# Optimization experiments

Measured on AMD Instinct MI355X. Metric: run time of the kernel, lower is better.

Reference implementation:

```python
import jax, jax.numpy as jnp
import numpy as np

B, LQ, LK, D, H = 2, 1024, 1024, 1024, 16
DH = D // H


def setup_inputs() -> dict:
    key = jax.random.key(0)
    ks = jax.random.split(key, 14)
    s = 1.0 / np.sqrt(D)
    inp = {
        "q": jax.random.normal(ks[0], (B, LQ, D), jnp.float32),
        "k": jax.random.normal(ks[1], (B, LK, D), jnp.float32),
        "v": jax.random.normal(ks[2], (B, LK, D), jnp.float32),
        "Wq": jax.random.normal(ks[3], (D, D), jnp.float32) * s,
        "bq": jnp.zeros((D,), jnp.float32),
        "Wk": jax.random.normal(ks[4], (D, D), jnp.float32) * s,
        "bk": jnp.zeros((D,), jnp.float32),
        "Wv": jax.random.normal(ks[5], (D, D), jnp.float32) * s,
        "bv": jnp.zeros((D,), jnp.float32),
        "Wo": jax.random.normal(ks[6], (D, D), jnp.float32) * s,
        "bo": jnp.zeros((D,), jnp.float32),
        "logits_bias": jax.random.normal(ks[7], (B, LQ, LK), jnp.float32),
        "key_padding_mask": jax.random.randint(ks[8], (B, LK), 0, 2) > 0,
    }
    return inp


def _split_heads(x):
    b, l, _ = x.shape
    return x.reshape(b, l, H, DH).transpose(0, 2, 1, 3)  # [B,H,L,DH]


def reference(q, k, v, Wq, bq, Wk, bk, Wv, bv, Wo, bo, logits_bias, key_padding_mask):
    qh = _split_heads(q @ Wq.T + bq)  # [B,H,Lq,DH]
    kh = _split_heads(k @ Wk.T + bk)  # [B,H,Lk,DH]
    vh = _split_heads(v @ Wv.T + bv)  # [B,H,Lk,DH]

    neg = jnp.finfo(qh.dtype).min
    # attn_mask = logits_bias broadcast over heads, masked_fill at padded keys
    attn_mask = jnp.where(key_padding_mask[:, None, None, :],
                          neg, logits_bias[:, None, :, :])  # [B,1,Lq,Lk]

    scale = 1.0 / np.sqrt(DH)
    scores = jnp.einsum('bhqd,bhkd->bhqk', qh, kh) * scale + attn_mask
    probs = jax.nn.softmax(scores, axis=-1)
    out = jnp.einsum('bhqk,bhkd->bhqd', probs, vh)  # [B,H,Lq,DH]
    out = out.transpose(0, 2, 1, 3).reshape(q.shape[0], q.shape[1], D)
    return out @ Wo.T + bo
```

## Files before the change

### kernel.cpp

```cpp
#include <hip/hip_runtime.h>


typedef _Float16 half8 __attribute__((ext_vector_type(8)));
typedef _Float16 half4_t __attribute__((ext_vector_type(4)));
typedef float f32x4 __attribute__((ext_vector_type(4)));

#define MFMA16(a, b, c) __builtin_amdgcn_mfma_f32_16x16x32_f16((a), (b), (c), 0, 0, 0)

#define WAITCNT_VM(n) asm volatile("s_waitcnt vmcnt(" #n ")" ::: "memory")
#define WAITCNT_LGKM0() asm volatile("s_waitcnt lgkmcnt(0)" ::: "memory")
#define RAW_BARRIER() asm volatile("s_barrier" ::: "memory")

__device__ __forceinline__ void gload16(const void* g, void* l) {
  __builtin_amdgcn_global_load_lds(
      (const __attribute__((address_space(1))) unsigned int*)g,
      (__attribute__((address_space(3))) unsigned int*)l, 16, 0, 0);
}

__device__ __forceinline__ half8 frag_ld(const _Float16* t, int row, int ck) {
  return *(const half8*)(t + row * 64 + (((ck ^ (row & 7)) << 3)));
}

__global__ __launch_bounds__(256) void cvt_f32_f16(
    const float* __restrict__ q, const float* __restrict__ k, const float* __restrict__ v,
    const float* __restrict__ Wq, const float* __restrict__ Wk,
    const float* __restrict__ Wv, const float* __restrict__ Wo,
    _Float16* __restrict__ q16, _Float16* __restrict__ k16, _Float16* __restrict__ v16,
    _Float16* __restrict__ w16) {
  const int y = blockIdx.y;
  if (y >= 3 && blockIdx.x >= 512) return;
  const float* s;
  _Float16* d;
  const size_t M = (size_t)1024 * 1024;
  switch (y) {
    case 0: s = q;  d = q16; break;
    case 1: s = k;  d = k16; break;
    case 2: s = v;  d = v16; break;
    case 3: s = Wq; d = w16; break;
    case 4: s = Wk; d = w16 + M; break;
    case 5: s = Wv; d = w16 + 2 * M; break;
    default: s = Wo; d = w16 + 3 * M; break;
  }
  const size_t i = ((size_t)blockIdx.x * 256 + threadIdx.x) * 8;
  const float4 a = *(const float4*)(s + i);
  const float4 bvv = *(const float4*)(s + i + 4);
  half8 h;
  h[0] = (_Float16)a.x; h[1] = (_Float16)a.y; h[2] = (_Float16)a.z; h[3] = (_Float16)a.w;
  h[4] = (_Float16)bvv.x; h[5] = (_Float16)bvv.y; h[6] = (_Float16)bvv.z; h[7] = (_Float16)bvv.w;
  *(half8*)(d + i) = h;
}

__global__ __launch_bounds__(256) void mmp(
    const _Float16* __restrict__ Aq, const _Float16* __restrict__ Ak,
    const _Float16* __restrict__ Av, const _Float16* __restrict__ W16,
    const float* __restrict__ c0, const float* __restrict__ c1,
    const float* __restrict__ c2, _Float16* __restrict__ Dq,
    _Float16* __restrict__ Dk, _Float16* __restrict__ Dvt,
    float* __restrict__ Df, int is_final) {
  __shared__ __align__(16) _Float16 lds[24576];

  const int tid = threadIdx.x;
  const int wv = tid >> 6, ln = tid & 63;
  const int quad = ln >> 4, col = ln & 15;
  const int wm = wv >> 1, wn = wv & 1;
  const int n0 = blockIdx.x * 128;
  const int m0 = blockIdx.y * 64;
  const int z = blockIdx.z;

  const _Float16* A = (z == 0) ? Aq : (z == 1) ? Ak : Av;
  const _Float16* Bw = W16 + (size_t)z * 1024 * 1024;
  const float* bias = (z == 0) ? c0 : (z == 1) ? c1 : c2;

  auto stage = [&](int buf, int k0) {
#pragma unroll
    for (int j = 0; j < 6; ++j) {
      const int ci = j * 256 + tid;
      const _Float16* src;
      if (ci < 512) {
        const int row = ci >> 3, lc = (ci & 7) ^ (row & 7);
        src = A + (size_t)(m0 + row) * 1024 + k0 + lc * 8;
      } else {
        const int di = ci - 512;
        const int row = di >> 3, lc = (di & 7) ^ (row & 7);
        src = Bw + (size_t)(n0 + row) * 1024 + k0 + lc * 8;
      }
      gload16(src, lds + buf * 12288 + (j * 256 + wv * 64) * 8);
    }
  };

  const f32x4 zero4 = {0.f, 0.f, 0.f, 0.f};
  f32x4 acc[2][4];
#pragma unroll
  for (int i = 0; i < 2; ++i)
#pragma unroll
    for (int j = 0; j < 4; ++j) acc[i][j] = zero4;

  stage(0, 0);
  for (int i = 0; i < 15; ++i) {
    stage((i + 1) & 1, (i + 1) * 64);
    WAITCNT_VM(6);
    RAW_BARRIER();
    const _Float16* As = lds + (i & 1) * 12288;
    const _Float16* Bs = As + 4096;
    half8 af[2][2], bf[2][4];
#pragma unroll
    for (int kk = 0; kk < 2; ++kk) {
#pragma unroll
      for (int mi = 0; mi < 2; ++mi)
        af[kk][mi] = frag_ld(As, wm * 32 + mi * 16 + col, kk * 4 + quad);
#pragma unroll
      for (int ni = 0; ni < 4; ++ni)
        bf[kk][ni] = frag_ld(Bs, wn * 64 + ni * 16 + col, kk * 4 + quad);
    }
    WAITCNT_LGKM0();
    RAW_BARRIER();
#pragma unroll
    for (int kk = 0; kk < 2; ++kk)
#pragma unroll
      for (int mi = 0; mi < 2; ++mi)
#pragma unroll
        for (int ni = 0; ni < 4; ++ni)
          acc[mi][ni] = MFMA16(af[kk][mi], bf[kk][ni], acc[mi][ni]);
  }
  {
    WAITCNT_VM(0);
    RAW_BARRIER();
    const _Float16* As = lds + 12288;
    const _Float16* Bs = As + 4096;
#pragma unroll
    for (int kk = 0; kk < 2; ++kk) {
      half8 af[2], bf[4];
#pragma unroll
      for (int mi = 0; mi < 2; ++mi)
        af[mi] = frag_ld(As, wm * 32 + mi * 16 + col, kk * 4 + quad);
#pragma unroll
      for (int ni = 0; ni < 4; ++ni)
        bf[ni] = frag_ld(Bs, wn * 64 + ni * 16 + col, kk * 4 + quad);
#pragma unroll
      for (int mi = 0; mi < 2; ++mi)
#pragma unroll
        for (int ni = 0; ni < 4; ++ni)
          acc[mi][ni] = MFMA16(af[mi], bf[ni], acc[mi][ni]);
    }
  }

  float bv[4];
#pragma unroll
  for (int ni = 0; ni < 4; ++ni) bv[ni] = bias[n0 + wn * 64 + ni * 16 + col];

  if (is_final) {
#pragma unroll
    for (int mi = 0; mi < 2; ++mi) {
      const int m_g = m0 + wm * 32 + mi * 16 + quad * 4;
#pragma unroll
      for (int ni = 0; ni < 4; ++ni) {
        const int n_g = n0 + wn * 64 + ni * 16 + col;
#pragma unroll
        for (int r = 0; r < 4; ++r)
          Df[(size_t)(m_g + r) * 1024 + n_g] = acc[mi][ni][r] + bv[ni];
      }
    }
  } else if (z < 2) {
    _Float16* D = z ? Dk : Dq;
#pragma unroll
    for (int mi = 0; mi < 2; ++mi) {
      const int m_g = m0 + wm * 32 + mi * 16 + quad * 4;
#pragma unroll
      for (int ni = 0; ni < 4; ++ni) {
        const int n_g = n0 + wn * 64 + ni * 16 + col;
        const int h = n_g >> 6, dh = n_g & 63;
#pragma unroll
        for (int r = 0; r < 4; ++r) {
          const int b = (m_g + r) >> 10, l = (m_g + r) & 1023;
          D[((size_t)((b * 16 + h) * 1024) + l) * 64 + dh] =
              (_Float16)(acc[mi][ni][r] + bv[ni]);
        }
      }
    }
  } else {
    __syncthreads();
    _Float16* Ct = lds;
#pragma unroll
    for (int mi = 0; mi < 2; ++mi) {
      const int ml = wm * 32 + mi * 16 + quad * 4;
#pragma unroll
      for (int ni = 0; ni < 4; ++ni) {
        const int nl = wn * 64 + ni * 16 + col;
#pragma unroll
        for (int r = 0; r < 4; ++r)
          Ct[(size_t)nl * 72 + ml + r] = (_Float16)(acc[mi][ni][r] + bv[ni]);
      }
    }
    __syncthreads();
#pragma unroll
    for (int it = 0; it < 4; ++it) {
      const int ci = it * 256 + tid;
      const int n = ci >> 3;
      const int mc = (ci & 7) * 8;
      const half8 hv = *(const half8*)(Ct + (size_t)n * 72 + mc);
      const int n_g = n0 + n;
      const int h = n_g >> 6, dh = n_g & 63;
      const int m_g = m0 + mc;
      const int b = m_g >> 10, l = m_g & 1023;
      *(half8*)(Dvt + ((size_t)((b * 16 + h) * 64 + dh)) * 1024 + l) = hv;
    }
  }
}

__global__ __launch_bounds__(256) void attn(
    const _Float16* __restrict__ Qh, const _Float16* __restrict__ Kh,
    const _Float16* __restrict__ Vt, const float* __restrict__ biasL,
    const int* __restrict__ kpm, _Float16* __restrict__ AO) {
  __shared__ __align__(16) _Float16 KV[2 * 16384];
  __shared__ __align__(16) _Float16 Pt[4][1024];

  const int tid = threadIdx.x;
  const int wv = tid >> 6, ln = tid & 63;
  const int quad = ln >> 4, col = ln & 15;
  const int qsub = wv & 1, khalf = wv >> 1;
  const int q0 = blockIdx.x * 32;
  const int bh = blockIdx.y;
  const int b = bh >> 4, hh = bh & 15;
  const int qg = q0 + qsub * 16 + col;

  const _Float16* Qp = Qh + ((size_t)bh * 1024 + qg) * 64;
  const half8 bq0 = *(const half8*)(Qp + quad * 8);
  const half8 bq1 = *(const half8*)(Qp + 32 + quad * 8);
  WAITCNT_VM(0);

  const float* biasRow = biasL + ((size_t)(b * 1024 + qg)) * 1024;
  const int* kpmRow = kpm + b * 1024;
  const int stage_kbase = (wv & 1) * 512;

  auto stageKV = [&](int buf, int it) {
    const int skoff = stage_kbase + it * 64;
#pragma unroll
    for (int j = 0; j < 8; ++j) {
      const int ci = j * 64 + ln;
      const int row = ci >> 3;
      const int lc = (ci & 7) ^ (row & 7);
      const void* src =
          (wv < 2) ? (const void*)(Kh + ((size_t)bh * 1024 + skoff + row) * 64 + lc * 8)
                   : (const void*)(Vt + ((size_t)bh * 64 + row) * 1024 + skoff + lc * 8);
      gload16(src, KV + buf * 16384 + wv * 4096 + j * 512);
    }
  };
  auto loadBias = [&](int it, f32x4* bb, int4* mk) {
    const int koff = khalf * 512 + it * 64;
#pragma unroll
    for (int mi = 0; mi < 4; ++mi) {
      const int kg = koff + mi * 16 + quad * 4;
      mk[mi] = *(const int4*)&kpmRow[kg];
      bb[mi] = *(const f32x4*)&biasRow[kg];
    }
  };

  const f32x4 zero4 = {0.f, 0.f, 0.f, 0.f};
  f32x4 o[4];
#pragma unroll
  for (int ni = 0; ni < 4; ++ni) o[ni] = zero4;
  float m_i = -1e30f, l_i = 0.f;
  _Float16* Pw = Pt[wv];

  auto compute = [&](int buf, const f32x4* bb, const int4* mk) {
    const _Float16* Ks = KV + buf * 16384 + khalf * 4096;
    const _Float16* Vs = KV + buf * 16384 + (2 + khalf) * 4096;
    f32x4 s[4];
#pragma unroll
    for (int mi = 0; mi < 4; ++mi) {
      f32x4 a4 = zero4;
      a4 = MFMA16(frag_ld(Ks, mi * 16 + col, quad), bq0, a4);
      a4 = MFMA16(frag_ld(Ks, mi * 16 + col, 4 + quad), bq1, a4);
      s[mi] = a4;
    }
#pragma unroll
    for (int mi = 0; mi < 4; ++mi) {
      const int* mp = (const int*)&mk[mi];
#pragma unroll
      for (int r = 0; r < 4; ++r)
        s[mi][r] = mp[r] ? -1e9f : s[mi][r] * 0.125f + bb[mi][r];
    }
    float rm = -1e30f;
#pragma unroll
    for (int mi = 0; mi < 4; ++mi)
#pragma unroll
      for (int r = 0; r < 4; ++r) rm = fmaxf(rm, s[mi][r]);
    rm = fmaxf(rm, __shfl_xor(rm, 16));
    rm = fmaxf(rm, __shfl_xor(rm, 32));
    const float mn = fmaxf(m_i, rm);
    const float alpha = __expf(m_i - mn);
    m_i = mn;
    float ps = 0.f;
#pragma unroll
    for (int mi = 0; mi < 4; ++mi)
#pragma unroll
      for (int r = 0; r < 4; ++r) {
        const float p = __expf(s[mi][r] - mn);
        s[mi][r] = p;
        ps += p;
      }
    ps += __shfl_xor(ps, 16);
    ps += __shfl_xor(ps, 32);
    l_i = l_i * alpha + ps;
#pragma unroll
    for (int ni = 0; ni < 4; ++ni)
#pragma unroll
      for (int r = 0; r < 4; ++r) o[ni][r] *= alpha;
#pragma unroll
    for (int mi = 0; mi < 4; ++mi) {
      half4_t h;
      h[0] = (_Float16)s[mi][0]; h[1] = (_Float16)s[mi][1];
      h[2] = (_Float16)s[mi][2]; h[3] = (_Float16)s[mi][3];
      const int kloc = mi * 16 + quad * 4;
      const int chunk = kloc >> 3;
      *(half4_t*)(Pw + col * 64 + (((chunk ^ (col & 7)) << 3) | (kloc & 7))) = h;
    }
    const half8 p0 = frag_ld(Pw, col, quad);
    const half8 p1 = frag_ld(Pw, col, 4 + quad);
#pragma unroll
    for (int ni = 0; ni < 4; ++ni) {
      o[ni] = MFMA16(frag_ld(Vs, ni * 16 + col, quad), p0, o[ni]);
      o[ni] = MFMA16(frag_ld(Vs, ni * 16 + col, 4 + quad), p1, o[ni]);
    }
  };

  f32x4 bbA[4], bbB[4];
  int4 mkA[4], mkB[4];
  stageKV(0, 0);
  loadBias(0, bbA, mkA);
  for (int i = 0; i < 7; ++i) {
    stageKV((i + 1) & 1, i + 1);
    loadBias(i + 1, bbB, mkB);
    WAITCNT_VM(16);
    RAW_BARRIER();
    compute(i & 1, bbA, mkA);
    WAITCNT_LGKM0();
    RAW_BARRIER();
#pragma unroll
    for (int mi = 0; mi < 4; ++mi) { bbA[mi] = bbB[mi]; mkA[mi] = mkB[mi]; }
  }
  WAITCNT_VM(0);
  RAW_BARRIER();
  compute(1, bbA, mkA);

  __syncthreads();
  f32x4* Ox = (f32x4*)&Pt[0][0];
  float* MlS = (float*)&KV[0];
  if (khalf == 1) {
#pragma unroll
    for (int ni = 0; ni < 4; ++ni) Ox[(qsub * 4 + ni) * 64 + ln] = o[ni];
    MlS[qsub * 64 + ln] = m_i;
    MlS[128 + qsub * 64 + ln] = l_i;
  }
  __syncthreads();
  if (khalf == 0) {
    const float m2 = MlS[qsub * 64 + ln];
    const float l2 = MlS[128 + qsub * 64 + ln];
    const float ms = fmaxf(m_i, m2);
    const float w1 = __expf(m_i - ms);
    const float w2 = __expf(m2 - ms);
    const float inv = 1.0f / (l_i * w1 + l2 * w2);
#pragma unroll
    for (int ni = 0; ni < 4; ++ni) {
      const f32x4 o2 = Ox[(qsub * 4 + ni) * 64 + ln];
      half4_t h;
#pragma unroll
      for (int r = 0; r < 4; ++r)
        h[r] = (_Float16)((o[ni][r] * w1 + o2[r] * w2) * inv);
      *(half4_t*)&AO[((size_t)(b * 1024 + qg)) * 1024 + hh * 64 + ni * 16 + quad * 4] = h;
    }
  }
}

extern "C" void kernel_launch(void* const* d_in, const int* in_sizes, int n_in,
                              void* d_out, int out_size, void* d_ws, size_t ws_size,
                              hipStream_t stream) {
  (void)in_sizes; (void)n_in; (void)out_size; (void)ws_size;
  const float* q = (const float*)d_in[0];
  const float* k = (const float*)d_in[1];
  const float* v = (const float*)d_in[2];
  const float* Wq = (const float*)d_in[3];
  const float* bq = (const float*)d_in[4];
  const float* Wk = (const float*)d_in[5];
  const float* bk = (const float*)d_in[6];
  const float* Wv = (const float*)d_in[7];
  const float* bv = (const float*)d_in[8];
  const float* Wo = (const float*)d_in[9];
  const float* bo = (const float*)d_in[10];
  const float* lb = (const float*)d_in[11];
  const int* kpm = (const int*)d_in[12];
  float* out = (float*)d_out;

  const size_t NT = (size_t)2 * 1024 * 1024;
  _Float16* q16 = (_Float16*)d_ws;
  _Float16* k16 = q16 + NT;
  _Float16* v16 = k16 + NT;
  _Float16* Qh = v16 + NT;
  _Float16* Kh = Qh + NT;
  _Float16* Vt = Kh + NT;
  _Float16* w16 = Vt + NT;
  _Float16* AO = q16;

  cvt_f32_f16<<<dim3(1024, 7), 256, 0, stream>>>(q, k, v, Wq, Wk, Wv, Wo,
                                                 q16, k16, v16, w16);
  mmp<<<dim3(8, 32, 3), 256, 0, stream>>>(q16, k16, v16, w16, bq, bk, bv,
                                          Qh, Kh, Vt, nullptr, 0);
  attn<<<dim3(32, 32), 256, 0, stream>>>(Qh, Kh, Vt, lb, kpm, AO);
  mmp<<<dim3(8, 32, 1), 256, 0, stream>>>(AO, nullptr, nullptr, w16 + 3 * NT / 2,
                                          bo, nullptr, nullptr, nullptr, nullptr,
                                          nullptr, out, 1);
}
```

Baseline: 177.5 us.

## Precompute fp16 masked bias in log2 domain and restructure attention to 512-thread blocks

Adds a pre-pass that folds the key-padding mask and a log2(e) scale into an fp16 bias tensor, so the attention loop reads half the bias bytes and no mask. Attention now uses exp2 with a pre-scaled QK factor. Blocks grow to 512 threads covering 64 queries, split keys within each 64-key tile, and share one K/V stage per iteration. The cost is an extra kernel pass over the full bias and fp16 rounding of the bias.

```diff
diff --git a/kernel.cpp b/kernel.cpp
--- a/kernel.cpp
+++ b/kernel.cpp
@@ -10,6 +10,7 @@
 #define WAITCNT_VM(n) asm volatile("s_waitcnt vmcnt(" #n ")" ::: "memory")
 #define WAITCNT_LGKM0() asm volatile("s_waitcnt lgkmcnt(0)" ::: "memory")
 #define RAW_BARRIER() asm volatile("s_barrier" ::: "memory")
+#define EXP2F(x) __builtin_amdgcn_exp2f(x)
 
 __device__ __forceinline__ void gload16(const void* g, void* l) {
   __builtin_amdgcn_global_load_lds(
@@ -50,6 +51,30 @@
   *(half8*)(d + i) = h;
 }
 
+__global__ __launch_bounds__(256) void cvt_bias(
+    const float* __restrict__ biasL, const int* __restrict__ kpm,
+    _Float16* __restrict__ biasC) {
+  const size_t i = ((size_t)blockIdx.x * 256 + threadIdx.x) * 8;
+  const int b = (int)(i >> 20);
+  const int kk = (int)(i & 1023);
+  const int* mrow = kpm + (b << 10) + kk;
+  const float4 b0 = *(const float4*)(biasL + i);
+  const float4 b1 = *(const float4*)(biasL + i + 4);
+  const int4 m0 = *(const int4*)mrow;
+  const int4 m1 = *(const int4*)(mrow + 4);
+  const float sc = 1.44269504f;
+  half8 h;
+  h[0] = m0.x ? (_Float16)-30000.f : (_Float16)(b0.x * sc);
+  h[1] = m0.y ? (_Float16)-30000.f : (_Float16)(b0.y * sc);
+  h[2] = m0.z ? (_Float16)-30000.f : (_Float16)(b0.z * sc);
+  h[3] = m0.w ? (_Float16)-30000.f : (_Float16)(b0.w * sc);
+  h[4] = m1.x ? (_Float16)-30000.f : (_Float16)(b1.x * sc);
+  h[5] = m1.y ? (_Float16)-30000.f : (_Float16)(b1.y * sc);
+  h[6] = m1.z ? (_Float16)-30000.f : (_Float16)(b1.z * sc);
+  h[7] = m1.w ? (_Float16)-30000.f : (_Float16)(b1.w * sc);
+  *(half8*)(biasC + i) = h;
+}
+
 __global__ __launch_bounds__(256) void mmp(
     const _Float16* __restrict__ Aq, const _Float16* __restrict__ Ak,
     const _Float16* __restrict__ Av, const _Float16* __restrict__ W16,
@@ -207,18 +232,18 @@
   }
 }
 
-__global__ __launch_bounds__(256) void attn(
+__global__ __launch_bounds__(512, 4) void attn(
     const _Float16* __restrict__ Qh, const _Float16* __restrict__ Kh,
-    const _Float16* __restrict__ Vt, const float* __restrict__ biasL,
-    const int* __restrict__ kpm, _Float16* __restrict__ AO) {
-  __shared__ __align__(16) _Float16 KV[2 * 16384];
-  __shared__ __align__(16) _Float16 Pt[4][1024];
+    const _Float16* __restrict__ Vt, const _Float16* __restrict__ biasC,
+    _Float16* __restrict__ AO) {
+  __shared__ __align__(16) _Float16 KV[2 * 8192];
+  __shared__ __align__(16) _Float16 Pt[8][512];
 
   const int tid = threadIdx.x;
   const int wv = tid >> 6, ln = tid & 63;
   const int quad = ln >> 4, col = ln & 15;
-  const int qsub = wv & 1, khalf = wv >> 1;
-  const int q0 = blockIdx.x * 32;
+  const int qsub = wv >> 1, khalf = wv & 1;
+  const int q0 = blockIdx.x * 64;
   const int bh = blockIdx.y;
   const int b = bh >> 4, hh = bh & 15;
   const int qg = q0 + qsub * 16 + col;
@@ -228,31 +253,30 @@
   const half8 bq1 = *(const half8*)(Qp + 32 + quad * 8);
   WAITCNT_VM(0);
 
-  const float* biasRow = biasL + ((size_t)(b * 1024 + qg)) * 1024;
-  const int* kpmRow = kpm + b * 1024;
-  const int stage_kbase = (wv & 1) * 512;
+  const _Float16* biasRow = biasC + ((size_t)(b * 1024 + qg)) * 1024;
 
   auto stageKV = [&](int buf, int it) {
-    const int skoff = stage_kbase + it * 64;
-#pragma unroll
-    for (int j = 0; j < 8; ++j) {
-      const int ci = j * 64 + ln;
-      const int row = ci >> 3;
-      const int lc = (ci & 7) ^ (row & 7);
-      const void* src =
-          (wv < 2) ? (const void*)(Kh + ((size_t)bh * 1024 + skoff + row) * 64 + lc * 8)
-                   : (const void*)(Vt + ((size_t)bh * 64 + row) * 1024 + skoff + lc * 8);
-      gload16(src, KV + buf * 16384 + wv * 4096 + j * 512);
+    const int koff = it * 64;
+#pragma unroll
+    for (int j = 0; j < 2; ++j) {
+      const int ci = j * 512 + tid;
+      const void* src;
+      if (ci < 512) {
+        const int row = ci >> 3, lc = (ci & 7) ^ (row & 7);
+        src = Kh + ((size_t)bh * 1024 + koff + row) * 64 + lc * 8;
+      } else {
+        const int di = ci - 512;
+        const int row = di >> 3, lc = (di & 7) ^ (row & 7);
+        src = Vt + ((size_t)bh * 64 + row) * 1024 + koff + lc * 8;
+      }
+      gload16(src, KV + buf * 8192 + (j * 512 + wv * 64) * 8);
     }
   };
-  auto loadBias = [&](int it, f32x4* bb, int4* mk) {
-    const int koff = khalf * 512 + it * 64;
-#pragma unroll
-    for (int mi = 0; mi < 4; ++mi) {
-      const int kg = koff + mi * 16 + quad * 4;
-      mk[mi] = *(const int4*)&kpmRow[kg];
-      bb[mi] = *(const f32x4*)&biasRow[kg];
-    }
+  auto loadBias = [&](int it, half4_t* bb) {
+    const int koff = it * 64 + khalf * 32;
+#pragma unroll
+    for (int mi = 0; mi < 2; ++mi)
+      bb[mi] = *(const half4_t*)&biasRow[koff + mi * 16 + quad * 4];
   };
 
   const f32x4 zero4 = {0.f, 0.f, 0.f, 0.f};
@@ -262,40 +286,35 @@
   float m_i = -1e30f, l_i = 0.f;
   _Float16* Pw = Pt[wv];
 
-  auto compute = [&](int buf, const f32x4* bb, const int4* mk) {
-    const _Float16* Ks = KV + buf * 16384 + khalf * 4096;
-    const _Float16* Vs = KV + buf * 16384 + (2 + khalf) * 4096;
-    f32x4 s[4];
-#pragma unroll
-    for (int mi = 0; mi < 4; ++mi) {
+  auto compute = [&](int buf, const half4_t* bb) {
+    const _Float16* Ks = KV + buf * 8192;
+    const _Float16* Vs = Ks + 4096;
+    f32x4 s[2];
+#pragma unroll
+    for (int mi = 0; mi < 2; ++mi) {
       f32x4 a4 = zero4;
-      a4 = MFMA16(frag_ld(Ks, mi * 16 + col, quad), bq0, a4);
-      a4 = MFMA16(frag_ld(Ks, mi * 16 + col, 4 + quad), bq1, a4);
+      a4 = MFMA16(frag_ld(Ks, khalf * 32 + mi * 16 + col, quad), bq0, a4);
+      a4 = MFMA16(frag_ld(Ks, khalf * 32 + mi * 16 + col, 4 + quad), bq1, a4);
       s[mi] = a4;
     }
 #pragma unroll
-    for (int mi = 0; mi < 4; ++mi) {
-      const int* mp = (const int*)&mk[mi];
+    for (int mi = 0; mi < 2; ++mi)
 #pragma unroll
       for (int r = 0; r < 4; ++r)
-        s[mi][r] = mp[r] ? -1e9f : s[mi][r] * 0.125f + bb[mi][r];
-    }
-    float rm = -1e30f;
-#pragma unroll
-    for (int mi = 0; mi < 4; ++mi)
-#pragma unroll
-      for (int r = 0; r < 4; ++r) rm = fmaxf(rm, s[mi][r]);
+        s[mi][r] = s[mi][r] * 0.18033688f + (float)bb[mi][r];
+    float rm = fmaxf(fmaxf(fmaxf(s[0][0], s[0][1]), fmaxf(s[0][2], s[0][3])),
+                     fmaxf(fmaxf(s[1][0], s[1][1]), fmaxf(s[1][2], s[1][3])));
     rm = fmaxf(rm, __shfl_xor(rm, 16));
     rm = fmaxf(rm, __shfl_xor(rm, 32));
     const float mn = fmaxf(m_i, rm);
-    const float alpha = __expf(m_i - mn);
+    const float alpha = EXP2F(m_i - mn);
     m_i = mn;
     float ps = 0.f;
 #pragma unroll
-    for (int mi = 0; mi < 4; ++mi)
+    for (int mi = 0; mi < 2; ++mi)
 #pragma unroll
       for (int r = 0; r < 4; ++r) {
-        const float p = __expf(s[mi][r] - mn);
+        const float p = EXP2F(s[mi][r] - mn);
         s[mi][r] = p;
         ps += p;
       }
@@ -307,58 +326,52 @@
 #pragma unroll
       for (int r = 0; r < 4; ++r) o[ni][r] *= alpha;
 #pragma unroll
-    for (int mi = 0; mi < 4; ++mi) {
+    for (int mi = 0; mi < 2; ++mi) {
       half4_t h;
       h[0] = (_Float16)s[mi][0]; h[1] = (_Float16)s[mi][1];
       h[2] = (_Float16)s[mi][2]; h[3] = (_Float16)s[mi][3];
       const int kloc = mi * 16 + quad * 4;
-      const int chunk = kloc >> 3;
-      *(half4_t*)(Pw + col * 64 + (((chunk ^ (col & 7)) << 3) | (kloc & 7))) = h;
-    }
-    const half8 p0 = frag_ld(Pw, col, quad);
-    const half8 p1 = frag_ld(Pw, col, 4 + quad);
-#pragma unroll
-    for (int ni = 0; ni < 4; ++ni) {
-      o[ni] = MFMA16(frag_ld(Vs, ni * 16 + col, quad), p0, o[ni]);
-      o[ni] = MFMA16(frag_ld(Vs, ni * 16 + col, 4 + quad), p1, o[ni]);
-    }
+      *(half4_t*)(Pw + col * 32 + ((((kloc >> 3) ^ (col & 3)) << 3) | (kloc & 7))) = h;
+    }
+    const half8 p0 = *(const half8*)(Pw + col * 32 + ((quad ^ (col & 3)) << 3));
+#pragma unroll
+    for (int ni = 0; ni < 4; ++ni)
+      o[ni] = MFMA16(frag_ld(Vs, ni * 16 + col, khalf * 4 + quad), p0, o[ni]);
   };
 
-  f32x4 bbA[4], bbB[4];
-  int4 mkA[4], mkB[4];
+  half4_t bbA[2], bbB[2];
   stageKV(0, 0);
-  loadBias(0, bbA, mkA);
-  for (int i = 0; i < 7; ++i) {
+  loadBias(0, bbA);
+  for (int i = 0; i < 15; ++i) {
     stageKV((i + 1) & 1, i + 1);
-    loadBias(i + 1, bbB, mkB);
-    WAITCNT_VM(16);
+    loadBias(i + 1, bbB);
+    WAITCNT_VM(4);
     RAW_BARRIER();
-    compute(i & 1, bbA, mkA);
+    compute(i & 1, bbA);
     WAITCNT_LGKM0();
     RAW_BARRIER();
-#pragma unroll
-    for (int mi = 0; mi < 4; ++mi) { bbA[mi] = bbB[mi]; mkA[mi] = mkB[mi]; }
+    bbA[0] = bbB[0]; bbA[1] = bbB[1];
   }
   WAITCNT_VM(0);
   RAW_BARRIER();
-  compute(1, bbA, mkA);
+  compute(1, bbA);
 
   __syncthreads();
-  f32x4* Ox = (f32x4*)&Pt[0][0];
-  float* MlS = (float*)&KV[0];
+  f32x4* Ox = (f32x4*)&KV[0];
+  float* MlS = (float*)&KV[8192];
   if (khalf == 1) {
 #pragma unroll
     for (int ni = 0; ni < 4; ++ni) Ox[(qsub * 4 + ni) * 64 + ln] = o[ni];
     MlS[qsub * 64 + ln] = m_i;
-    MlS[128 + qsub * 64 + ln] = l_i;
+    MlS[256 + qsub * 64 + ln] = l_i;
   }
   __syncthreads();
   if (khalf == 0) {
     const float m2 = MlS[qsub * 64 + ln];
-    const float l2 = MlS[128 + qsub * 64 + ln];
+    const float l2 = MlS[256 + qsub * 64 + ln];
     const float ms = fmaxf(m_i, m2);
-    const float w1 = __expf(m_i - ms);
-    const float w2 = __expf(m2 - ms);
+    const float w1 = EXP2F(m_i - ms);
+    const float w2 = EXP2F(m2 - ms);
     const float inv = 1.0f / (l_i * w1 + l2 * w2);
 #pragma unroll
     for (int ni = 0; ni < 4; ++ni) {
@@ -400,12 +413,14 @@
   _Float16* Vt = Kh + NT;
   _Float16* w16 = Vt + NT;
   _Float16* AO = q16;
+  _Float16* biasC = k16;
 
   cvt_f32_f16<<<dim3(1024, 7), 256, 0, stream>>>(q, k, v, Wq, Wk, Wv, Wo,
                                                  q16, k16, v16, w16);
   mmp<<<dim3(8, 32, 3), 256, 0, stream>>>(q16, k16, v16, w16, bq, bk, bv,
                                           Qh, Kh, Vt, nullptr, 0);
-  attn<<<dim3(32, 32), 256, 0, stream>>>(Qh, Kh, Vt, lb, kpm, AO);
+  cvt_bias<<<dim3(1024), 256, 0, stream>>>(lb, kpm, biasC);
+  attn<<<dim3(16, 32), 512, 0, stream>>>(Qh, Kh, Vt, biasC, AO);
   mmp<<<dim3(8, 32, 1), 256, 0, stream>>>(AO, nullptr, nullptr, w16 + 3 * NT / 2,
                                           bo, nullptr, nullptr, nullptr, nullptr,
                                           nullptr, out, 1);
```

Result: no change. 174.1 us (-2.0%).
